# Kernel optimization log

Measured on AMD Instinct MI355X. Metric: run time of the kernel, lower is better.

The kernel has to match this reference:

```python
import jax, jax.numpy as jnp
import numpy as np

DIM = 4096
N_HEADS = 32
HEAD_DIM = DIM // N_HEADS
BATCH = 2
SEQ = 1024
THETA = 10000.0
NEG_INF = -1e9


def _rope_cos_sin(seq_len, head_dim):
    # NOTE: original code constructs RotatePosEmbedding with config.dim but applies
    # it per-head; the only shape-consistent interpretation (standard Llama RoPE)
    # uses head_dim frequencies, which is what we implement.
    inv_freq = 1.0 / (THETA ** (jnp.arange(0, head_dim, 2, dtype=jnp.float32) / head_dim))
    angles = jnp.arange(seq_len, dtype=jnp.float32)[:, None] * inv_freq[None, :]  # [S, hd/2]
    return jnp.cos(angles), jnp.sin(angles)


def _apply_rope(x, cos, sin):
    # x: [B,S,H,hd]; rotate consecutive pairs (complex multiply)
    B, S, H, hd = x.shape
    xr = x.reshape(B, S, H, hd // 2, 2)
    x0, x1 = xr[..., 0], xr[..., 1]
    c = cos[None, :, None, :]
    s = sin[None, :, None, :]
    out = jnp.stack([x0 * c - x1 * s, x0 * s + x1 * c], axis=-1)
    return out.reshape(B, S, H, hd)


def setup_inputs() -> dict:
    key = jax.random.key(0)
    ks = jax.random.split(key, 9)
    x = jax.random.normal(ks[0], (BATCH, SEQ, DIM), dtype=jnp.float32)
    scale = 1.0 / np.sqrt(DIM)
    wq = jax.random.normal(ks[1], (DIM, DIM), dtype=jnp.float32) * scale
    wk = jax.random.normal(ks[2], (DIM, DIM), dtype=jnp.float32) * scale
    wv = jax.random.normal(ks[3], (DIM, DIM), dtype=jnp.float32) * scale
    wo = jax.random.normal(ks[4], (DIM, DIM), dtype=jnp.float32) * scale
    bq = jax.random.normal(ks[5], (DIM,), dtype=jnp.float32) * 0.01
    bk = jax.random.normal(ks[6], (DIM,), dtype=jnp.float32) * 0.01
    bv = jax.random.normal(ks[7], (DIM,), dtype=jnp.float32) * 0.01
    bo = jax.random.normal(ks[8], (DIM,), dtype=jnp.float32) * 0.01
    # causal additive mask [S,S]
    mask = jnp.where(jnp.tril(jnp.ones((SEQ, SEQ), dtype=bool)), 0.0, NEG_INF).astype(jnp.float32)
    return {"x": x, "wq": wq, "bq": bq, "wk": wk, "bk": bk, "wv": wv, "bv": bv,
            "wo": wo, "bo": bo, "mask": mask, "start_pos": 0}


def reference(x, wq, bq, wk, bk, wv, bv, wo, bo, mask, start_pos):
    B, S, D = x.shape
    H, hd = N_HEADS, D // N_HEADS
    q = (x @ wq.T + bq).reshape(B, S, H, hd)
    k = (x @ wk.T + bk).reshape(B, S, H, hd)
    v = (x @ wv.T + bv).reshape(B, S, H, hd)
    cos, sin = _rope_cos_sin(S, hd)
    q = _apply_rope(q, cos, sin)
    k = _apply_rope(k, cos, sin)
    # start_pos == 0 prefill: cache slice [:start_pos+S] equals current k/v
    scores = jnp.einsum('bqhd,bkhd->bhqk', q, k) / np.sqrt(hd).astype(np.float32)
    scores = scores + mask[None, None, :, :]
    attn = jax.nn.softmax(scores, axis=-1)
    out = jnp.einsum('bhqk,bkhd->bqhd', attn, v).reshape(B, S, D)
    return out @ wo.T + bo
```

## Files before the change

### kernel.cpp

```cpp
#include <hip/hip_runtime.h>
#include <hip/hip_bf16.h>

#define DIM   4096
#define NH    32
#define HD    128
#define BATCH 2
#define SEQ   1024
#define MROWS (BATCH*SEQ)
#define LDQ   12288

typedef __attribute__((ext_vector_type(8))) short bf16x8;
typedef __attribute__((ext_vector_type(4))) short s16x4;
typedef __attribute__((ext_vector_type(4))) float f32x4;

__device__ inline void gload_lds16(const void* g, void* l) {
  __builtin_amdgcn_global_load_lds(
      (const __attribute__((address_space(1))) void*)g,
      (__attribute__((address_space(3))) void*)l, 16, 0, 0);
}

__device__ inline float bf2f(short b) {
  unsigned u = ((unsigned)(unsigned short)b) << 16;
  return __uint_as_float(u);
}
__device__ inline unsigned short f2bfu(float f) {
  __hip_bfloat16 h = __float2bfloat16(f);
  return *reinterpret_cast<unsigned short*>(&h);
}

__global__ void cvt_bf16_kernel(const float* __restrict__ in,
                                unsigned short* __restrict__ out, long n4) {
  long i = blockIdx.x * (long)blockDim.x + threadIdx.x;
  long stride = (long)gridDim.x * blockDim.x;
  for (; i < n4; i += stride) {
    float4 v = ((const float4*)in)[i];
    ushort4 o;
    o.x = f2bfu(v.x); o.y = f2bfu(v.y); o.z = f2bfu(v.z); o.w = f2bfu(v.w);
    ((ushort4*)out)[i] = o;
  }
}

__global__ void concat3_kernel(const float* __restrict__ a, const float* __restrict__ b,
                               const float* __restrict__ c, float* __restrict__ o) {
  int i = blockIdx.x * blockDim.x + threadIdx.x;
  if (i < 4096) o[i] = a[i];
  else if (i < 8192) o[i] = b[i - 4096];
  else if (i < 12288) o[i] = c[i - 8192];
}

__global__ void rope_table_kernel(float* __restrict__ cosT, float* __restrict__ sinT) {
  int s = blockIdx.x;
  int p = threadIdx.x;
  float inv = powf(10000.0f, -((float)(2 * p)) / 128.0f);
  float a = (float)s * inv;
  cosT[s * 64 + p] = cosf(a);
  sinT[s * 64 + p] = sinf(a);
}

__global__ void rope_apply_kernel(unsigned short* __restrict__ qkv,
                                  const float* __restrict__ cosT,
                                  const float* __restrict__ sinT) {
  int c = blockIdx.x * blockDim.x + threadIdx.x;
  long e = (long)c * 8;
  int row = (int)(e >> 13);
  int col = (int)(e & 8191);
  int s = row & (SEQ - 1);
  int d = col & (HD - 1);
  int p0 = d >> 1;
  unsigned short* p = qkv + (size_t)row * LDQ + col;
  bf16x8 v = *(bf16x8*)p;
  f32x4 cv = *(const f32x4*)&cosT[s * 64 + p0];
  f32x4 sv = *(const f32x4*)&sinT[s * 64 + p0];
  bf16x8 o;
#pragma unroll
  for (int j = 0; j < 4; ++j) {
    float x0 = bf2f(v[2 * j]);
    float x1 = bf2f(v[2 * j + 1]);
    o[2 * j]     = (short)f2bfu(x0 * cv[j] - x1 * sv[j]);
    o[2 * j + 1] = (short)f2bfu(x0 * sv[j] + x1 * cv[j]);
  }
  *(bf16x8*)p = o;
}

__device__ __forceinline__ void stage_tile(
    const unsigned short* __restrict__ A, const unsigned short* __restrict__ Bw,
    unsigned short* Asl, unsigned short* Bsl,
    int m0, int n0, int K, int kbase, int t) {
#pragma unroll
  for (int j = 0; j < 4; ++j) {
    int ci = j * 512 + t;
    int r = ci >> 3, c = ci & 7;
    gload_lds16(A + (size_t)(m0 + r) * K + kbase + ((c ^ (r & 7)) << 3), Asl + ci * 8);
  }
#pragma unroll
  for (int j = 0; j < 2; ++j) {
    int ci = j * 512 + t;
    int r = ci >> 3, c = ci & 7;
    gload_lds16(Bw + (size_t)(n0 + r) * K + kbase + ((c ^ (r & 7)) << 3), Bsl + ci * 8);
  }
}

template <typename OutT>
__global__ __launch_bounds__(512, 2) void gemm_bt_p_kernel(
    const unsigned short* __restrict__ A, const unsigned short* __restrict__ Bw,
    const float* __restrict__ bias, OutT* __restrict__ C, int M, int N, int K) {
  __shared__ unsigned short As[2][256 * 64];
  __shared__ unsigned short Bs[2][128 * 64];
  const int t = threadIdx.x;
  const int lane = t & 63;
  const int w = t >> 6;
  const int wm = w >> 2, wn = w & 3;
  const int np = lane & 15, hq = lane >> 4;

  int bid = blockIdx.y * gridDim.x + blockIdx.x;
  int nwg = gridDim.x * gridDim.y;
  int sb = (bid & 7) * (nwg >> 3) + (bid >> 3);
  int bx = sb % gridDim.x, by = sb / gridDim.x;
  const int m0 = by * 256, n0 = bx * 128;
  const int NT = K >> 6;

  stage_tile(A, Bw, As[0], Bs[0], m0, n0, K, 0, t);
  stage_tile(A, Bw, As[1], Bs[1], m0, n0, K, 64, t);

  f32x4 acc[8][2] = {};

  asm volatile("s_waitcnt vmcnt(6)" ::: "memory");
  __builtin_amdgcn_s_barrier();

  int cur = 0;
  for (int kt = 0; kt < NT; ++kt) {
    const unsigned short* Asl = As[cur];
    const unsigned short* Bsl = Bs[cur];
    bf16x8 a0[8], b0[2];
#pragma unroll
    for (int i = 0; i < 8; ++i)
      a0[i] = *(const bf16x8*)&Asl[(wm * 128 + i * 16 + np) * 64 + ((hq ^ (np & 7)) << 3)];
#pragma unroll
    for (int j = 0; j < 2; ++j)
      b0[j] = *(const bf16x8*)&Bsl[(wn * 32 + j * 16 + np) * 64 + ((hq ^ (np & 7)) << 3)];
    __builtin_amdgcn_s_setprio(1);
#pragma unroll
    for (int i = 0; i < 8; ++i)
#pragma unroll
      for (int j = 0; j < 2; ++j)
        acc[i][j] = __builtin_amdgcn_mfma_f32_16x16x32_bf16(a0[i], b0[j], acc[i][j], 0, 0, 0);
    __builtin_amdgcn_s_setprio(0);
    bf16x8 a1[8], b1[2];
#pragma unroll
    for (int i = 0; i < 8; ++i)
      a1[i] = *(const bf16x8*)&Asl[(wm * 128 + i * 16 + np) * 64 + (((4 + hq) ^ (np & 7)) << 3)];
#pragma unroll
    for (int j = 0; j < 2; ++j)
      b1[j] = *(const bf16x8*)&Bsl[(wn * 32 + j * 16 + np) * 64 + (((4 + hq) ^ (np & 7)) << 3)];
    asm volatile("s_waitcnt lgkmcnt(0)" ::: "memory");
    __builtin_amdgcn_s_barrier();
    if (kt + 2 < NT)
      stage_tile(A, Bw, As[cur], Bs[cur], m0, n0, K, (kt + 2) << 6, t);
    __builtin_amdgcn_s_setprio(1);
#pragma unroll
    for (int i = 0; i < 8; ++i)
#pragma unroll
      for (int j = 0; j < 2; ++j)
        acc[i][j] = __builtin_amdgcn_mfma_f32_16x16x32_bf16(a1[i], b1[j], acc[i][j], 0, 0, 0);
    __builtin_amdgcn_s_setprio(0);
    if (kt + 2 < NT) {
      asm volatile("s_waitcnt vmcnt(6)" ::: "memory");
    } else {
      asm volatile("s_waitcnt vmcnt(0)" ::: "memory");
    }
    __builtin_amdgcn_s_barrier();
    cur ^= 1;
  }

  const int orow0 = m0 + wm * 128 + hq * 4;
  const int ocol0 = n0 + wn * 32 + np;
#pragma unroll
  for (int j = 0; j < 2; ++j) {
    float bj = bias[ocol0 + j * 16];
#pragma unroll
    for (int i = 0; i < 8; ++i) {
#pragma unroll
      for (int r = 0; r < 4; ++r) {
        float v = acc[i][j][r] + bj;
        size_t off = (size_t)(orow0 + i * 16 + r) * N + (ocol0 + j * 16);
        if constexpr (sizeof(OutT) == 2)
          ((unsigned short*)C)[off] = f2bfu(v);
        else
          ((float*)C)[off] = v;
      }
    }
  }
}

__global__ __launch_bounds__(256, 1) void flash_attn_kernel(
    const unsigned short* __restrict__ QKV, unsigned short* __restrict__ O) {
  __shared__ unsigned short Ks[64 * 128];
  __shared__ unsigned short Vt[128 * 64];
  __shared__ unsigned short Ps[4][32 * 64];

  const int p  = blockIdx.x;
  const int bh = blockIdx.y;
  const int b  = bh >> 5;
  const int hh = bh & 31;
  const int t    = threadIdx.x;
  const int lane = t & 63;
  const int w    = t >> 6;
  const int np   = lane & 15;
  const int hq   = lane >> 4;

  const size_t rowbase = (size_t)b * SEQ * LDQ;
  const unsigned short* Qg = QKV + rowbase + (size_t)hh * HD;
  const unsigned short* Kg = QKV + rowbase + 4096 + (size_t)hh * HD;
  const unsigned short* Vg = QKV + rowbase + 8192 + (size_t)hh * HD;
  unsigned short* Og = O + (size_t)b * SEQ * DIM + (size_t)hh * HD;

  const int krow = t >> 2;
  const int kc0  = (t & 3) * 32;
  const int vr0  = (t & 15) * 4;
  const int vc0  = (t >> 4) * 8;

  unsigned short* Pw = &Ps[w][0];
  const float SCALE = 0.08838834764831843f;

  bf16x8 vk[4], vv[4];

#pragma unroll 1
  for (int pass = 0; pass < 2; ++pass) {
    const int qt    = pass ? (7 - p) : p;
    const int nt    = 2 * qt + 2;
    const int qbase = qt * 128 + w * 32;

    bf16x8 qf[2][4];
#pragma unroll
    for (int rb = 0; rb < 2; ++rb)
#pragma unroll
      for (int kb = 0; kb < 4; ++kb)
        qf[rb][kb] = *(const bf16x8*)&Qg[(size_t)(qbase + rb * 16 + np) * LDQ + kb * 32 + hq * 8];

    f32x4 acc[2][8] = {};
    float m_run[2][4], l_run[2][4];
#pragma unroll
    for (int rb = 0; rb < 2; ++rb)
#pragma unroll
      for (int r = 0; r < 4; ++r) { m_run[rb][r] = -3.0e38f; l_run[rb][r] = 0.0f; }

    {
      const unsigned short* kp = Kg + (size_t)krow * LDQ + kc0;
      const unsigned short* vp = Vg + (size_t)vr0 * LDQ + vc0;
#pragma unroll
      for (int jj = 0; jj < 4; ++jj) vk[jj] = *(const bf16x8*)(kp + jj * 8);
#pragma unroll
      for (int jj = 0; jj < 4; ++jj) vv[jj] = *(const bf16x8*)(vp + (size_t)jj * LDQ);
    }

#pragma unroll 1
    for (int kt = 0; kt < nt; ++kt) {
      __syncthreads();

#pragma unroll
      for (int jj = 0; jj < 4; ++jj) {
        int c = (t & 3) * 4 + jj;
        *(bf16x8*)((char*)Ks + krow * 256 + ((c ^ (krow & 7)) << 4)) = vk[jj];
      }
#pragma unroll
      for (int i = 0; i < 8; ++i) {
        int col = vc0 + i;
        s16x4 sv;
        sv[0] = vv[0][i]; sv[1] = vv[1][i]; sv[2] = vv[2][i]; sv[3] = vv[3][i];
        *(s16x4*)((char*)Vt + ((col * 128 + vr0 * 2) ^ ((col & 7) << 4))) = sv;
      }
      __syncthreads();

      if (kt + 1 < nt) {
        const unsigned short* kp = Kg + (size_t)((kt + 1) * 64 + krow) * LDQ + kc0;
        const unsigned short* vp = Vg + (size_t)((kt + 1) * 64 + vr0) * LDQ + vc0;
#pragma unroll
        for (int jj = 0; jj < 4; ++jj) vk[jj] = *(const bf16x8*)(kp + jj * 8);
#pragma unroll
        for (int jj = 0; jj < 4; ++jj) vv[jj] = *(const bf16x8*)(vp + (size_t)jj * LDQ);
      }

      f32x4 sc[4][2] = {};
#pragma unroll
      for (int ct = 0; ct < 4; ++ct) {
#pragma unroll
        for (int kb = 0; kb < 4; ++kb) {
          bf16x8 kf = *(const bf16x8*)((char*)Ks + (ct * 16 + np) * 256 +
                                       (((kb * 4 + hq) ^ (np & 7)) << 4));
          sc[ct][0] = __builtin_amdgcn_mfma_f32_16x16x32_bf16(qf[0][kb], kf, sc[ct][0], 0, 0, 0);
          sc[ct][1] = __builtin_amdgcn_mfma_f32_16x16x32_bf16(qf[1][kb], kf, sc[ct][1], 0, 0, 0);
        }
      }

      const bool maskt = (kt >= 2 * qt);
#pragma unroll
      for (int ct = 0; ct < 4; ++ct) {
        int kvc = kt * 64 + ct * 16 + np;
#pragma unroll
        for (int rb = 0; rb < 2; ++rb)
#pragma unroll
          for (int r = 0; r < 4; ++r) {
            float v = sc[ct][rb][r] * SCALE;
            if (maskt && kvc > qbase + rb * 16 + hq * 4 + r) v = -1.0e9f;
            sc[ct][rb][r] = v;
          }
      }

      float sf[2][4];
#pragma unroll
      for (int rb = 0; rb < 2; ++rb)
#pragma unroll
        for (int r = 0; r < 4; ++r) {
          float tmax = fmaxf(fmaxf(sc[0][rb][r], sc[1][rb][r]),
                             fmaxf(sc[2][rb][r], sc[3][rb][r]));
          tmax = fmaxf(tmax, __shfl_xor(tmax, 1));
          tmax = fmaxf(tmax, __shfl_xor(tmax, 2));
          tmax = fmaxf(tmax, __shfl_xor(tmax, 4));
          tmax = fmaxf(tmax, __shfl_xor(tmax, 8));
          float mn = fmaxf(m_run[rb][r], tmax);
          sf[rb][r] = __expf(m_run[rb][r] - mn);
          m_run[rb][r] = mn;
        }

#pragma unroll
      for (int rb = 0; rb < 2; ++rb)
#pragma unroll
        for (int r = 0; r < 4; ++r) {
          int prow = rb * 16 + hq * 4 + r;
          int swz = (prow & 7) << 4;
          float rsum = 0.f;
#pragma unroll
          for (int ct = 0; ct < 4; ++ct) {
            float pv = __expf(sc[ct][rb][r] - m_run[rb][r]);
            rsum += pv;
            *(unsigned short*)((char*)Pw + ((prow * 128 + (ct * 16 + np) * 2) ^ swz)) = f2bfu(pv);
          }
          rsum += __shfl_xor(rsum, 1);
          rsum += __shfl_xor(rsum, 2);
          rsum += __shfl_xor(rsum, 4);
          rsum += __shfl_xor(rsum, 8);
          l_run[rb][r] = l_run[rb][r] * sf[rb][r] + rsum;
        }

#pragma unroll
      for (int rb = 0; rb < 2; ++rb)
#pragma unroll
        for (int nt2 = 0; nt2 < 8; ++nt2)
#pragma unroll
          for (int r = 0; r < 4; ++r)
            acc[rb][nt2][r] *= sf[rb][r];

#pragma unroll
      for (int kb2 = 0; kb2 < 2; ++kb2) {
        bf16x8 pa0 = *(const bf16x8*)((char*)Pw +
            (((0 * 16 + np) * 128 + kb2 * 64 + hq * 16) ^ ((np & 7) << 4)));
        bf16x8 pa1 = *(const bf16x8*)((char*)Pw +
            (((1 * 16 + np) * 128 + kb2 * 64 + hq * 16) ^ ((np & 7) << 4)));
#pragma unroll
        for (int nt2 = 0; nt2 < 8; ++nt2) {
          int col = nt2 * 16 + np;
          bf16x8 vf = *(const bf16x8*)((char*)Vt +
              ((col * 128 + kb2 * 64 + hq * 16) ^ ((col & 7) << 4)));
          acc[0][nt2] = __builtin_amdgcn_mfma_f32_16x16x32_bf16(pa0, vf, acc[0][nt2], 0, 0, 0);
          acc[1][nt2] = __builtin_amdgcn_mfma_f32_16x16x32_bf16(pa1, vf, acc[1][nt2], 0, 0, 0);
        }
      }
    }

#pragma unroll
    for (int rb = 0; rb < 2; ++rb)
#pragma unroll
      for (int r = 0; r < 4; ++r) {
        float rl = 1.0f / l_run[rb][r];
        int orow = qbase + rb * 16 + hq * 4 + r;
#pragma unroll
        for (int nt2 = 0; nt2 < 8; ++nt2)
          Og[(size_t)orow * DIM + nt2 * 16 + np] = f2bfu(acc[rb][nt2][r] * rl);
      }
  }
}

extern "C" void kernel_launch(void* const* d_in, const int* in_sizes, int n_in,
                              void* d_out, int out_size, void* d_ws, size_t ws_size,
                              hipStream_t stream) {
  const float* x  = (const float*)d_in[0];
  const float* wq = (const float*)d_in[1];
  const float* bq = (const float*)d_in[2];
  const float* wk = (const float*)d_in[3];
  const float* bk = (const float*)d_in[4];
  const float* wv = (const float*)d_in[5];
  const float* bv = (const float*)d_in[6];
  const float* wo = (const float*)d_in[7];
  const float* bo = (const float*)d_in[8];
  float* out = (float*)d_out;

  char* ws = (char*)d_ws;
  unsigned short* wqkvb = (unsigned short*)(ws);
  unsigned short* wob   = (unsigned short*)(ws + (96ll  << 20));
  unsigned short* xb    = (unsigned short*)(ws + (128ll << 20));
  unsigned short* qkv   = (unsigned short*)(ws + (144ll << 20));
  unsigned short* ab    = (unsigned short*)(ws + (192ll << 20));
  float* biasqkv = (float*)(ws + (208ll << 20));
  float* cosT    = (float*)(ws + (208ll << 20) + (64  << 10));
  float* sinT    = (float*)(ws + (208ll << 20) + (320 << 10));

  cvt_bf16_kernel<<<2048, 256, 0, stream>>>(x,  xb, (long)MROWS * DIM / 4);
  cvt_bf16_kernel<<<2048, 256, 0, stream>>>(wq, wqkvb,                       (long)DIM * DIM / 4);
  cvt_bf16_kernel<<<2048, 256, 0, stream>>>(wk, wqkvb + (size_t)DIM * DIM,   (long)DIM * DIM / 4);
  cvt_bf16_kernel<<<2048, 256, 0, stream>>>(wv, wqkvb + 2 * (size_t)DIM * DIM,(long)DIM * DIM / 4);
  cvt_bf16_kernel<<<2048, 256, 0, stream>>>(wo, wob, (long)DIM * DIM / 4);

  concat3_kernel<<<48, 256, 0, stream>>>(bq, bk, bv, biasqkv);
  rope_table_kernel<<<SEQ, 64, 0, stream>>>(cosT, sinT);

  dim3 gq(LDQ / 128, MROWS / 256);
  gemm_bt_p_kernel<unsigned short><<<gq, 512, 0, stream>>>(xb, wqkvb, biasqkv, qkv,
                                                           MROWS, LDQ, DIM);

  rope_apply_kernel<<<(MROWS * 8192 / 8) / 256, 256, 0, stream>>>(qkv, cosT, sinT);

  dim3 ga(4, BATCH * NH);
  flash_attn_kernel<<<ga, 256, 0, stream>>>(qkv, ab);

  dim3 go(DIM / 128, MROWS / 256);
  gemm_bt_p_kernel<float><<<go, 512, 0, stream>>>(ab, wob, bo, out, MROWS, DIM, DIM);
}
```

Measured before the change: 560.1 us.

## Enlarge GEMM tile to 256x256, fuse RoPE into QKV epilogue, split-K output projection

The GEMM kernel now uses a 256x256 output tile per workgroup, with a quarter-staged load and MFMA schedule, so each loaded tile is reused across more outputs. RoPE is applied in the QKV GEMM epilogue through a lane shuffle between paired columns, which removes the separate rope_apply pass over Q and K. The output projection is split along K into two partial fp32 results, then a reduce kernel adds them and the bias, to put more workgroups on the device. The costs are extra register and LDS pressure, an extra fp32 partial buffer that aliases the weight workspace, and one more kernel launch.

```diff
diff --git a/kernel.cpp b/kernel.cpp
--- a/kernel.cpp
+++ b/kernel.cpp
@@ -57,55 +57,46 @@
   sinT[s * 64 + p] = sinf(a);
 }
 
-__global__ void rope_apply_kernel(unsigned short* __restrict__ qkv,
-                                  const float* __restrict__ cosT,
-                                  const float* __restrict__ sinT) {
-  int c = blockIdx.x * blockDim.x + threadIdx.x;
-  long e = (long)c * 8;
-  int row = (int)(e >> 13);
-  int col = (int)(e & 8191);
-  int s = row & (SEQ - 1);
-  int d = col & (HD - 1);
-  int p0 = d >> 1;
-  unsigned short* p = qkv + (size_t)row * LDQ + col;
-  bf16x8 v = *(bf16x8*)p;
-  f32x4 cv = *(const f32x4*)&cosT[s * 64 + p0];
-  f32x4 sv = *(const f32x4*)&sinT[s * 64 + p0];
-  bf16x8 o;
-#pragma unroll
-  for (int j = 0; j < 4; ++j) {
-    float x0 = bf2f(v[2 * j]);
-    float x1 = bf2f(v[2 * j + 1]);
-    o[2 * j]     = (short)f2bfu(x0 * cv[j] - x1 * sv[j]);
-    o[2 * j + 1] = (short)f2bfu(x0 * sv[j] + x1 * cv[j]);
-  }
-  *(bf16x8*)p = o;
-}
-
-__device__ __forceinline__ void stage_tile(
+__global__ void reduce_bias_kernel(const float* __restrict__ part,
+                                   const float* __restrict__ bias,
+                                   float* __restrict__ out) {
+  long i = blockIdx.x * (long)blockDim.x + threadIdx.x;
+  if (i >= (long)MROWS * DIM / 4) return;
+  float4 a = ((const float4*)part)[i];
+  float4 b = ((const float4*)(part + (size_t)MROWS * DIM))[i];
+  float4 bb = ((const float4*)bias)[(int)(i & (DIM / 4 - 1))];
+  float4 o;
+  o.x = a.x + b.x + bb.x; o.y = a.y + b.y + bb.y;
+  o.z = a.z + b.z + bb.z; o.w = a.w + b.w + bb.w;
+  ((float4*)out)[i] = o;
+}
+
+__device__ __forceinline__ void stage_half(
     const unsigned short* __restrict__ A, const unsigned short* __restrict__ Bw,
     unsigned short* Asl, unsigned short* Bsl,
-    int m0, int n0, int K, int kbase, int t) {
-#pragma unroll
-  for (int j = 0; j < 4; ++j) {
-    int ci = j * 512 + t;
+    int m0, int n0, size_t Kstr, int kcol0, int t, int half) {
+#pragma unroll
+  for (int j = 0; j < 2; ++j) {
+    int ci = (half * 2 + j) * 512 + t;
     int r = ci >> 3, c = ci & 7;
-    gload_lds16(A + (size_t)(m0 + r) * K + kbase + ((c ^ (r & 7)) << 3), Asl + ci * 8);
+    gload_lds16(A + (size_t)(m0 + r) * Kstr + kcol0 + ((c ^ (r & 7)) << 3), Asl + ci * 8);
   }
 #pragma unroll
   for (int j = 0; j < 2; ++j) {
-    int ci = j * 512 + t;
+    int ci = (half * 2 + j) * 512 + t;
     int r = ci >> 3, c = ci & 7;
-    gload_lds16(Bw + (size_t)(n0 + r) * K + kbase + ((c ^ (r & 7)) << 3), Bsl + ci * 8);
-  }
-}
-
-template <typename OutT>
-__global__ __launch_bounds__(512, 2) void gemm_bt_p_kernel(
+    gload_lds16(Bw + (size_t)(n0 + r) * Kstr + kcol0 + ((c ^ (r & 7)) << 3), Bsl + ci * 8);
+  }
+}
+
+template <typename OutT, bool QKV_MODE>
+__global__ __launch_bounds__(512, 2) void gemm_q_kernel(
     const unsigned short* __restrict__ A, const unsigned short* __restrict__ Bw,
-    const float* __restrict__ bias, OutT* __restrict__ C, int M, int N, int K) {
+    const float* __restrict__ bias, OutT* __restrict__ C,
+    int M, int N, int Kstr, int Klen,
+    const float* __restrict__ cosT, const float* __restrict__ sinT) {
   __shared__ unsigned short As[2][256 * 64];
-  __shared__ unsigned short Bs[2][128 * 64];
+  __shared__ unsigned short Bs[2][128 * 64 * 2];
   const int t = threadIdx.x;
   const int lane = t & 63;
   const int w = t >> 6;
@@ -116,55 +107,104 @@
   int nwg = gridDim.x * gridDim.y;
   int sb = (bid & 7) * (nwg >> 3) + (bid >> 3);
   int bx = sb % gridDim.x, by = sb / gridDim.x;
-  const int m0 = by * 256, n0 = bx * 128;
-  const int NT = K >> 6;
-
-  stage_tile(A, Bw, As[0], Bs[0], m0, n0, K, 0, t);
-  stage_tile(A, Bw, As[1], Bs[1], m0, n0, K, 64, t);
-
-  f32x4 acc[8][2] = {};
-
-  asm volatile("s_waitcnt vmcnt(6)" ::: "memory");
+  const int m0 = by * 256, n0 = bx * 256;
+  const int kb0 = blockIdx.z * Klen;
+  const int NT = Klen >> 6;
+  OutT* Cz = C + (size_t)blockIdx.z * M * N;
+
+  stage_half(A, Bw, As[0], Bs[0], m0, n0, Kstr, kb0, t, 0);
+  stage_half(A, Bw, As[0], Bs[0], m0, n0, Kstr, kb0, t, 1);
+  stage_half(A, Bw, As[1], Bs[1], m0, n0, Kstr, kb0 + 64, t, 0);
+  stage_half(A, Bw, As[1], Bs[1], m0, n0, Kstr, kb0 + 64, t, 1);
+
+  f32x4 acc[8][4] = {};
+
+  asm volatile("s_waitcnt vmcnt(8)" ::: "memory");
   __builtin_amdgcn_s_barrier();
 
   int cur = 0;
+#pragma unroll 1
   for (int kt = 0; kt < NT; ++kt) {
     const unsigned short* Asl = As[cur];
     const unsigned short* Bsl = Bs[cur];
-    bf16x8 a0[8], b0[2];
-#pragma unroll
-    for (int i = 0; i < 8; ++i)
-      a0[i] = *(const bf16x8*)&Asl[(wm * 128 + i * 16 + np) * 64 + ((hq ^ (np & 7)) << 3)];
-#pragma unroll
-    for (int j = 0; j < 2; ++j)
-      b0[j] = *(const bf16x8*)&Bsl[(wn * 32 + j * 16 + np) * 64 + ((hq ^ (np & 7)) << 3)];
+    bf16x8 af[4][2], bf[4][2];
+    const int swz = np & 7;
+
+#pragma unroll
+    for (int rb = 0; rb < 4; ++rb)
+#pragma unroll
+      for (int kh = 0; kh < 2; ++kh)
+        af[rb][kh] = *(const bf16x8*)&Asl[(wm * 128 + rb * 16 + np) * 64 +
+                                          (((kh * 4 + hq) ^ swz) << 3)];
+#pragma unroll
+    for (int cb = 0; cb < 2; ++cb)
+#pragma unroll
+      for (int kh = 0; kh < 2; ++kh)
+        bf[cb][kh] = *(const bf16x8*)&Bsl[(wn * 64 + cb * 16 + np) * 64 +
+                                          (((kh * 4 + hq) ^ swz) << 3)];
+    __builtin_amdgcn_s_barrier();
     __builtin_amdgcn_s_setprio(1);
 #pragma unroll
-    for (int i = 0; i < 8; ++i)
-#pragma unroll
-      for (int j = 0; j < 2; ++j)
-        acc[i][j] = __builtin_amdgcn_mfma_f32_16x16x32_bf16(a0[i], b0[j], acc[i][j], 0, 0, 0);
+    for (int i = 0; i < 4; ++i)
+#pragma unroll
+      for (int j = 0; j < 2; ++j) {
+        acc[i][j] = __builtin_amdgcn_mfma_f32_16x16x32_bf16(af[i][0], bf[j][0], acc[i][j], 0, 0, 0);
+        acc[i][j] = __builtin_amdgcn_mfma_f32_16x16x32_bf16(af[i][1], bf[j][1], acc[i][j], 0, 0, 0);
+      }
     __builtin_amdgcn_s_setprio(0);
-    bf16x8 a1[8], b1[2];
-#pragma unroll
-    for (int i = 0; i < 8; ++i)
-      a1[i] = *(const bf16x8*)&Asl[(wm * 128 + i * 16 + np) * 64 + (((4 + hq) ^ (np & 7)) << 3)];
-#pragma unroll
-    for (int j = 0; j < 2; ++j)
-      b1[j] = *(const bf16x8*)&Bsl[(wn * 32 + j * 16 + np) * 64 + (((4 + hq) ^ (np & 7)) << 3)];
+
+#pragma unroll
+    for (int cb = 2; cb < 4; ++cb)
+#pragma unroll
+      for (int kh = 0; kh < 2; ++kh)
+        bf[cb][kh] = *(const bf16x8*)&Bsl[(wn * 64 + cb * 16 + np) * 64 +
+                                          (((kh * 4 + hq) ^ swz) << 3)];
+    __builtin_amdgcn_s_barrier();
+    __builtin_amdgcn_s_setprio(1);
+#pragma unroll
+    for (int i = 0; i < 4; ++i)
+#pragma unroll
+      for (int j = 0; j < 2; ++j) {
+        acc[i][j + 2] = __builtin_amdgcn_mfma_f32_16x16x32_bf16(af[i][0], bf[j + 2][0], acc[i][j + 2], 0, 0, 0);
+        acc[i][j + 2] = __builtin_amdgcn_mfma_f32_16x16x32_bf16(af[i][1], bf[j + 2][1], acc[i][j + 2], 0, 0, 0);
+      }
+    __builtin_amdgcn_s_setprio(0);
+
+#pragma unroll
+    for (int rb = 0; rb < 4; ++rb)
+#pragma unroll
+      for (int kh = 0; kh < 2; ++kh)
+        af[rb][kh] = *(const bf16x8*)&Asl[(wm * 128 + 64 + rb * 16 + np) * 64 +
+                                          (((kh * 4 + hq) ^ swz) << 3)];
     asm volatile("s_waitcnt lgkmcnt(0)" ::: "memory");
+    __builtin_amdgcn_sched_barrier(0);
     __builtin_amdgcn_s_barrier();
     if (kt + 2 < NT)
-      stage_tile(A, Bw, As[cur], Bs[cur], m0, n0, K, (kt + 2) << 6, t);
+      stage_half(A, Bw, As[cur], Bs[cur], m0, n0, Kstr, kb0 + ((kt + 2) << 6), t, 0);
     __builtin_amdgcn_s_setprio(1);
 #pragma unroll
-    for (int i = 0; i < 8; ++i)
-#pragma unroll
-      for (int j = 0; j < 2; ++j)
-        acc[i][j] = __builtin_amdgcn_mfma_f32_16x16x32_bf16(a1[i], b1[j], acc[i][j], 0, 0, 0);
+    for (int i = 0; i < 4; ++i)
+#pragma unroll
+      for (int j = 0; j < 2; ++j) {
+        acc[i + 4][j] = __builtin_amdgcn_mfma_f32_16x16x32_bf16(af[i][0], bf[j][0], acc[i + 4][j], 0, 0, 0);
+        acc[i + 4][j] = __builtin_amdgcn_mfma_f32_16x16x32_bf16(af[i][1], bf[j][1], acc[i + 4][j], 0, 0, 0);
+      }
+    __builtin_amdgcn_s_setprio(0);
+
+    if (kt + 2 < NT)
+      stage_half(A, Bw, As[cur], Bs[cur], m0, n0, Kstr, kb0 + ((kt + 2) << 6), t, 1);
+    __builtin_amdgcn_s_barrier();
+    __builtin_amdgcn_s_setprio(1);
+#pragma unroll
+    for (int i = 0; i < 4; ++i)
+#pragma unroll
+      for (int j = 0; j < 2; ++j) {
+        acc[i + 4][j + 2] = __builtin_amdgcn_mfma_f32_16x16x32_bf16(af[i][0], bf[j + 2][0], acc[i + 4][j + 2], 0, 0, 0);
+        acc[i + 4][j + 2] = __builtin_amdgcn_mfma_f32_16x16x32_bf16(af[i][1], bf[j + 2][1], acc[i + 4][j + 2], 0, 0, 0);
+      }
     __builtin_amdgcn_s_setprio(0);
     if (kt + 2 < NT) {
-      asm volatile("s_waitcnt vmcnt(6)" ::: "memory");
+      asm volatile("s_waitcnt vmcnt(8)" ::: "memory");
     } else {
       asm volatile("s_waitcnt vmcnt(0)" ::: "memory");
     }
@@ -172,21 +212,33 @@
     cur ^= 1;
   }
 
-  const int orow0 = m0 + wm * 128 + hq * 4;
-  const int ocol0 = n0 + wn * 32 + np;
-#pragma unroll
-  for (int j = 0; j < 2; ++j) {
-    float bj = bias[ocol0 + j * 16];
+  const int orow0 = m0 + wm * 128;
+  const int ocol0 = n0 + wn * 64 + np;
+  const bool do_rope = QKV_MODE && (n0 < 8192);
+#pragma unroll
+  for (int j = 0; j < 4; ++j) {
+    const int col = ocol0 + j * 16;
+    float bj = QKV_MODE ? bias[col] : 0.0f;
+    const int p0 = (col & 127) >> 1;
+    const bool even = (lane & 1) == 0;
 #pragma unroll
     for (int i = 0; i < 8; ++i) {
 #pragma unroll
       for (int r = 0; r < 4; ++r) {
+        int orow = orow0 + i * 16 + hq * 4 + r;
         float v = acc[i][j][r] + bj;
-        size_t off = (size_t)(orow0 + i * 16 + r) * N + (ocol0 + j * 16);
+        if (do_rope) {
+          int srow = orow & (SEQ - 1);
+          float c = cosT[srow * 64 + p0];
+          float s = sinT[srow * 64 + p0];
+          float pv = __shfl_xor(v, 1);
+          v = even ? (v * c - pv * s) : (pv * s + v * c);
+        }
+        size_t off = (size_t)orow * N + col;
         if constexpr (sizeof(OutT) == 2)
-          ((unsigned short*)C)[off] = f2bfu(v);
+          ((unsigned short*)Cz)[off] = f2bfu(v);
         else
-          ((float*)C)[off] = v;
+          ((float*)Cz)[off] = v;
       }
     }
   }
@@ -396,6 +448,7 @@
 
   char* ws = (char*)d_ws;
   unsigned short* wqkvb = (unsigned short*)(ws);
+  float* part           = (float*)(ws);
   unsigned short* wob   = (unsigned short*)(ws + (96ll  << 20));
   unsigned short* xb    = (unsigned short*)(ws + (128ll << 20));
   unsigned short* qkv   = (unsigned short*)(ws + (144ll << 20));
@@ -405,23 +458,24 @@
   float* sinT    = (float*)(ws + (208ll << 20) + (320 << 10));
 
   cvt_bf16_kernel<<<2048, 256, 0, stream>>>(x,  xb, (long)MROWS * DIM / 4);
-  cvt_bf16_kernel<<<2048, 256, 0, stream>>>(wq, wqkvb,                       (long)DIM * DIM / 4);
-  cvt_bf16_kernel<<<2048, 256, 0, stream>>>(wk, wqkvb + (size_t)DIM * DIM,   (long)DIM * DIM / 4);
+  cvt_bf16_kernel<<<2048, 256, 0, stream>>>(wq, wqkvb,                        (long)DIM * DIM / 4);
+  cvt_bf16_kernel<<<2048, 256, 0, stream>>>(wk, wqkvb + (size_t)DIM * DIM,    (long)DIM * DIM / 4);
   cvt_bf16_kernel<<<2048, 256, 0, stream>>>(wv, wqkvb + 2 * (size_t)DIM * DIM,(long)DIM * DIM / 4);
   cvt_bf16_kernel<<<2048, 256, 0, stream>>>(wo, wob, (long)DIM * DIM / 4);
 
   concat3_kernel<<<48, 256, 0, stream>>>(bq, bk, bv, biasqkv);
   rope_table_kernel<<<SEQ, 64, 0, stream>>>(cosT, sinT);
 
-  dim3 gq(LDQ / 128, MROWS / 256);
-  gemm_bt_p_kernel<unsigned short><<<gq, 512, 0, stream>>>(xb, wqkvb, biasqkv, qkv,
-                                                           MROWS, LDQ, DIM);
-
-  rope_apply_kernel<<<(MROWS * 8192 / 8) / 256, 256, 0, stream>>>(qkv, cosT, sinT);
+  dim3 gq(LDQ / 256, MROWS / 256, 1);
+  gemm_q_kernel<unsigned short, true><<<gq, 512, 0, stream>>>(
+      xb, wqkvb, biasqkv, qkv, MROWS, LDQ, DIM, DIM, cosT, sinT);
 
   dim3 ga(4, BATCH * NH);
   flash_attn_kernel<<<ga, 256, 0, stream>>>(qkv, ab);
 
-  dim3 go(DIM / 128, MROWS / 256);
-  gemm_bt_p_kernel<float><<<go, 512, 0, stream>>>(ab, wob, bo, out, MROWS, DIM, DIM);
-}
+  dim3 go(DIM / 256, MROWS / 256, 2);
+  gemm_q_kernel<float, false><<<go, 512, 0, stream>>>(
+      ab, wob, nullptr, part, MROWS, DIM, DIM, DIM / 2, nullptr, nullptr);
+
+  reduce_bias_kernel<<<(MROWS * DIM / 4 + 255) / 256, 256, 0, stream>>>(part, bo, out);
+}
```

Result: no change. 567.2 us (+1.3%).
